# Kernel tuning notes

Hardware: AMD Instinct MI355X
Metric: run time of the kernel (lower is better)

Reference implementation:

```python
import jax, jax.numpy as jnp
import numpy as np

# Fixed architecture constants from AlgelogicNetwork.__init__
M, J, I, L, W = 4, 2, 3, 2, 9
B = 1048576  # batch size (only free dim)


def setup_inputs() -> dict:
    key = jax.random.key(0)
    ks = jax.random.split(key, 7)
    state = jax.random.normal(ks[0], (B, W * L), dtype=jnp.float32)
    # rule.constants ~ U(-1, 1), rule.gammas ~ U(0, 1), stacked over M rules
    constants = jax.random.uniform(ks[1], (M, J, L), minval=-1.0, maxval=1.0, dtype=jnp.float32)
    gammas = jax.random.uniform(ks[2], (M, J, L), dtype=jnp.float32)
    # body Linears (L -> I), one per (rule m, premise j); head Linear (I -> L) per rule
    W_body = jax.random.normal(ks[3], (M, J, I, L), dtype=jnp.float32) * 0.5
    b_body = jax.random.normal(ks[4], (M, J, I), dtype=jnp.float32) * 0.1
    W_head = jax.random.normal(ks[5], (M, L, I), dtype=jnp.float32) * 0.5
    b_head = jax.random.normal(ks[6], (M, L), dtype=jnp.float32) * 0.1
    return {
        "state": state,
        "constants": constants,
        "gammas": gammas,
        "W_body": W_body,
        "b_body": b_body,
        "W_head": W_head,
        "b_head": b_head,
    }


def reference(state, constants, gammas, W_body, b_body, W_head, b_head):
    s = state.reshape(-1, W, L)                       # [B, W, L]
    g = jnp.clip(gammas, 0.0, 1.0)                    # sigmoid() in source = clamp; [M, J, L]
    wgt = 1.0 - g                                     # [M, J, L]

    # match_scores[m,j,b,w] = sum_l (1-g[m,j,l]) * (const[m,j,l] - s[b,w,l])^2
    # L=2 fixed: unroll over l to avoid a [M,J,B,W,L] intermediate
    ms = sum(
        wgt[:, :, l, None, None]
        * (constants[:, :, l, None, None] - s[None, None, :, :, l]) ** 2
        for l in range(L)
    )                                                  # [M, J, B, W]

    attn = jax.nn.softmax(-ms, axis=-1)                # softmax over W positions (temperature=1)
    best = jnp.einsum('mjbw,bwl->mjbl', attn, s)       # soft-gathered propositions
    match_quality = jnp.sum(attn * ms, axis=-1).sum(axis=1)   # [M, B], summed over premises j

    captured = jnp.einsum('mjbl,mjil->mjbi', best, W_body) + b_body[:, :, None, :]  # body Linear
    g_avg = g.mean(axis=-1)                            # [M, J]
    captured_vars = jnp.einsum('mj,mjbi->mbi', g_avg, captured)                     # [M, B, I]

    rule_out = jnp.einsum('mbi,mli->mbl', captured_vars, W_head) + b_head[:, None, :]  # [M, B, L]

    # similarity[m,b,w] = -sum_l (rule_out[m,b,l] - s[b,w,l])^2
    sim = -jnp.sum((rule_out[:, :, None, :] - s[None]) ** 2, axis=-1)  # [M, B, W]
    confidence = jnp.exp(-match_quality)               # [M, B]
    return jnp.einsum('mb,mbw->bw', confidence, sim)   # [B, W]
```

## Files before the change

### kernel.cpp

```cpp
#include <hip/hip_runtime.h>

namespace {
constexpr int kM = 4, kJ = 2, kI = 3, kL = 2, kW = 9;
constexpr float kInvLn2 = 1.4426950408889634f;

__device__ __forceinline__ float fexp2(float x) { return __builtin_amdgcn_exp2f(x); }

__global__ __launch_bounds__(256) void algelogic_one(
    const float* __restrict__ state,
    const float* __restrict__ constants,
    const float* __restrict__ gammas,
    const float* __restrict__ W_body,
    const float* __restrict__ b_body,
    const float* __restrict__ W_head,
    const float* __restrict__ b_head,
    float* __restrict__ out) {
  __shared__ float sdp[80];
  const int t = threadIdx.x;
  const int b = blockIdx.x * 256 + t;

  const float2* sr = reinterpret_cast<const float2*>(state) + (size_t)b * kW;
  float s0[kW], s1[kW];
#pragma unroll
  for (int w = 0; w < kW; ++w) {
    const float2 v = sr[w];
    s0[w] = v.x; s1[w] = v.y;
  }

  if (t < 8) {
    const int mj = t, m = t >> 1, j = t & 1;
    const float g0 = fminf(fmaxf(gammas[mj * kL + 0], 0.f), 1.f);
    const float g1 = fminf(fmaxf(gammas[mj * kL + 1], 0.f), 1.f);
    const float w0 = 1.f - g0, w1 = 1.f - g1;
    const float c0 = constants[mj * kL + 0], c1 = constants[mj * kL + 1];
    const float gavg = 0.5f * (g0 + g1);
    float* base = sdp + m * 20;
    base[0 + j] = -(w0 * c0 * c0 + w1 * c1 * c1) * kInvLn2;
    base[2 + j] = 2.f * w0 * c0 * kInvLn2;
    base[4 + j] = 2.f * w1 * c1 * kInvLn2;
    base[6 + j] = -w0 * kInvLn2;
    base[8 + j] = -w1 * kInvLn2;
#pragma unroll
    for (int l = 0; l < kL; ++l)
#pragma unroll
      for (int lp = 0; lp < kL; ++lp) {
        float acc = 0.f;
#pragma unroll
        for (int i = 0; i < kI; ++i)
          acc += W_head[(m * kL + l) * kI + i] * W_body[(mj * kI + i) * kL + lp];
        base[10 + (l * 2 + lp) * 2 + j] = gavg * acc;
      }
  } else if (t >= 64 && t < 68) {
    const int m = t - 64;
#pragma unroll
    for (int l = 0; l < kL; ++l) {
      float d = b_head[m * kL + l];
#pragma unroll
      for (int j = 0; j < kJ; ++j) {
        const int mj = m * kJ + j;
        const float g0 = fminf(fmaxf(gammas[mj * kL + 0], 0.f), 1.f);
        const float g1 = fminf(fmaxf(gammas[mj * kL + 1], 0.f), 1.f);
        const float gavg = 0.5f * (g0 + g1);
        float acc = 0.f;
#pragma unroll
        for (int i = 0; i < kI; ++i)
          acc += W_head[(m * kL + l) * kI + i] * b_body[mj * kI + i];
        d += gavg * acc;
      }
      sdp[m * 20 + 18 + l] = d;
    }
  }
  __syncthreads();

  float Cs = 0.f, X0 = 0.f, X1 = 0.f, K = 0.f;

#pragma unroll 1
  for (int m = 0; m < kM; ++m) {
    const float4* P4 = reinterpret_cast<const float4*>(sdp + m * 20);
    const float4 f0 = P4[0], f1 = P4[1], f2 = P4[2], f3 = P4[3], f4 = P4[4];

    float p0 = 1e-35f, p1 = 1e-35f;
    float a0 = 0.f, a1 = 0.f;
    float b0 = 0.f, b1 = 0.f;
    float g0 = 0.f, g1 = 0.f;
#pragma unroll
    for (int w = 0; w < kW; ++w) {
      const float sx = s0[w], sy = s1[w];
      float u = fmaf(f1.z, sx, f0.z);
      float mN0 = fmaf(u, sx, f0.x);
      float v = fmaf(f2.x, sy, f1.x);
      mN0 = fmaf(v, sy, mN0);
      const float e0 = fexp2(mN0);
      p0 += e0;
      a0 = fmaf(e0, sx, a0);
      b0 = fmaf(e0, sy, b0);
      g0 = fmaf(e0, mN0, g0);
      float u1 = fmaf(f1.w, sx, f0.w);
      float mN1 = fmaf(u1, sx, f0.y);
      float v1 = fmaf(f2.y, sy, f1.y);
      mN1 = fmaf(v1, sy, mN1);
      const float e1 = fexp2(mN1);
      p1 += e1;
      a1 = fmaf(e1, sx, a1);
      b1 = fmaf(e1, sy, b1);
      g1 = fmaf(e1, mN1, g1);
    }

    const float i0 = __builtin_amdgcn_rcpf(p0);
    const float i1 = __builtin_amdgcn_rcpf(p1);
    const float bb00 = a0 * i0, bb10 = b0 * i0;
    const float bb01 = a1 * i1, bb11 = b1 * i1;
    const float mq2 = fmaf(g0, i0, g1 * i1);
    const float conf = fexp2(mq2);

    float r0 = fmaf(f2.z, bb00, f4.z);
    r0 = fmaf(f3.x, bb10, r0);
    r0 = fmaf(f2.w, bb01, r0);
    r0 = fmaf(f3.y, bb11, r0);
    float r1 = fmaf(f3.z, bb00, f4.w);
    r1 = fmaf(f4.x, bb10, r1);
    r1 = fmaf(f3.w, bb01, r1);
    r1 = fmaf(f4.y, bb11, r1);

    Cs += conf;
    X0 = fmaf(conf, r0, X0);
    X1 = fmaf(conf, r1, X1);
    K = fmaf(conf, fmaf(r0, r0, r1 * r1), K);
  }

  const float X02 = 2.f * X0, X12 = 2.f * X1;
  float* orow = out + (size_t)b * kW;
#pragma unroll
  for (int w = 0; w < kW; ++w) {
    const float sx = s0[w], sy = s1[w];
    const float qs = fmaf(sx, sx, sy * sy);
    orow[w] = fmaf(X02, sx, fmaf(X12, sy, fmaf(-Cs, qs, -K)));
  }
}
}

extern "C" void kernel_launch(void* const* d_in, const int* in_sizes, int n_in,
                              void* d_out, int out_size, void* d_ws, size_t ws_size,
                              hipStream_t stream) {
  const float* state     = (const float*)d_in[0];
  const float* constants = (const float*)d_in[1];
  const float* gammas    = (const float*)d_in[2];
  const float* W_body    = (const float*)d_in[3];
  const float* b_body    = (const float*)d_in[4];
  const float* W_head    = (const float*)d_in[5];
  const float* b_head    = (const float*)d_in[6];
  float* out = (float*)d_out;

  const int B = in_sizes[0] / (kW * kL);
  hipLaunchKernelGGL(algelogic_one, dim3(B / 256), dim3(256), 0, stream,
                     state, constants, gammas, W_body, b_body, W_head, b_head, out);
}
```

Baseline: 32.92 us.

## Process two batch rows per thread with float4 loads and float2 stores

Each thread now handles a pair of batch rows, reading their 36 floats as nine float4 loads and writing outputs as float2 stores instead of float2 loads and scalar stores. The intent is wider memory transactions and half as many threads, so the per-block parameter setup is amortised over more work. In exchange, each thread holds more registers and the grid shrinks to half the blocks, which may reduce occupancy and latency hiding.

Result: slower. 37.42 us (+13.6%).

```diff
diff --git a/kernel.cpp b/kernel.cpp
--- a/kernel.cpp
+++ b/kernel.cpp
@@ -6,7 +6,7 @@
 
 __device__ __forceinline__ float fexp2(float x) { return __builtin_amdgcn_exp2f(x); }
 
-__global__ __launch_bounds__(256) void algelogic_one(
+__global__ __launch_bounds__(256) void algelogic_pair(
     const float* __restrict__ state,
     const float* __restrict__ constants,
     const float* __restrict__ gammas,
@@ -17,15 +17,12 @@
     float* __restrict__ out) {
   __shared__ float sdp[80];
   const int t = threadIdx.x;
-  const int b = blockIdx.x * 256 + t;
+  const size_t pi = (size_t)blockIdx.x * 256 + t;
 
-  const float2* sr = reinterpret_cast<const float2*>(state) + (size_t)b * kW;
-  float s0[kW], s1[kW];
+  const float4* sq = reinterpret_cast<const float4*>(state) + pi * 9;
+  float4 sF[9];
 #pragma unroll
-  for (int w = 0; w < kW; ++w) {
-    const float2 v = sr[w];
-    s0[w] = v.x; s1[w] = v.y;
-  }
+  for (int k = 0; k < 9; ++k) sF[k] = sq[k];
 
   if (t < 8) {
     const int mj = t, m = t >> 1, j = t & 1;
@@ -72,69 +69,98 @@
   }
   __syncthreads();
 
-  float Cs = 0.f, X0 = 0.f, X1 = 0.f, K = 0.f;
+  float Cs[2] = {0.f, 0.f}, X0[2] = {0.f, 0.f}, X1[2] = {0.f, 0.f},
+        K[2] = {0.f, 0.f};
 
 #pragma unroll 1
   for (int m = 0; m < kM; ++m) {
     const float4* P4 = reinterpret_cast<const float4*>(sdp + m * 20);
     const float4 f0 = P4[0], f1 = P4[1], f2 = P4[2], f3 = P4[3], f4 = P4[4];
 
-    float p0 = 1e-35f, p1 = 1e-35f;
-    float a0 = 0.f, a1 = 0.f;
-    float b0 = 0.f, b1 = 0.f;
-    float g0 = 0.f, g1 = 0.f;
+#pragma unroll
+    for (int elem = 0; elem < 2; ++elem) {
+      float p0 = 1e-35f, p1 = 1e-35f;
+      float a0 = 0.f, a1 = 0.f;
+      float b0 = 0.f, b1 = 0.f;
+      float q0 = 0.f, q1 = 0.f;
+#pragma unroll
+      for (int w = 0; w < kW; ++w) {
+        const int g = elem * 9 + w;
+        const float4 f = sF[g >> 1];
+        const float sx = (g & 1) ? f.z : f.x;
+        const float sy = (g & 1) ? f.w : f.y;
+        float u = fmaf(f1.z, sx, f0.z);
+        float mN0 = fmaf(u, sx, f0.x);
+        float v = fmaf(f2.x, sy, f1.x);
+        mN0 = fmaf(v, sy, mN0);
+        const float e0 = fexp2(mN0);
+        p0 += e0;
+        a0 = fmaf(e0, sx, a0);
+        b0 = fmaf(e0, sy, b0);
+        q0 = fmaf(e0, mN0, q0);
+        float u1 = fmaf(f1.w, sx, f0.w);
+        float mN1 = fmaf(u1, sx, f0.y);
+        float v1 = fmaf(f2.y, sy, f1.y);
+        mN1 = fmaf(v1, sy, mN1);
+        const float e1 = fexp2(mN1);
+        p1 += e1;
+        a1 = fmaf(e1, sx, a1);
+        b1 = fmaf(e1, sy, b1);
+        q1 = fmaf(e1, mN1, q1);
+      }
+
+      const float i0 = __builtin_amdgcn_rcpf(p0);
+      const float i1 = __builtin_amdgcn_rcpf(p1);
+      const float bb00 = a0 * i0, bb10 = b0 * i0;
+      const float bb01 = a1 * i1, bb11 = b1 * i1;
+      const float mq2 = fmaf(q0, i0, q1 * i1);
+      const float conf = fexp2(mq2);
+
+      float r0 = fmaf(f2.z, bb00, f4.z);
+      r0 = fmaf(f3.x, bb10, r0);
+      r0 = fmaf(f2.w, bb01, r0);
+      r0 = fmaf(f3.y, bb11, r0);
+      float r1 = fmaf(f3.z, bb00, f4.w);
+      r1 = fmaf(f4.x, bb10, r1);
+      r1 = fmaf(f3.w, bb01, r1);
+      r1 = fmaf(f4.y, bb11, r1);
+
+      Cs[elem] += conf;
+      X0[elem] = fmaf(conf, r0, X0[elem]);
+      X1[elem] = fmaf(conf, r1, X1[elem]);
+      K[elem] = fmaf(conf, fmaf(r0, r0, r1 * r1), K[elem]);
+    }
+  }
+
+  float* orow = out + pi * (2 * kW);
+#pragma unroll
+  for (int elem = 0; elem < 2; ++elem) {
+    const float X02 = 2.f * X0[elem], X12 = 2.f * X1[elem];
+    const float Csl = Cs[elem], Kl = K[elem];
+    float o[kW];
 #pragma unroll
     for (int w = 0; w < kW; ++w) {
-      const float sx = s0[w], sy = s1[w];
-      float u = fmaf(f1.z, sx, f0.z);
-      float mN0 = fmaf(u, sx, f0.x);
-      float v = fmaf(f2.x, sy, f1.x);
-      mN0 = fmaf(v, sy, mN0);
-      const float e0 = fexp2(mN0);
-      p0 += e0;
-      a0 = fmaf(e0, sx, a0);
-      b0 = fmaf(e0, sy, b0);
-      g0 = fmaf(e0, mN0, g0);
-      float u1 = fmaf(f1.w, sx, f0.w);
-      float mN1 = fmaf(u1, sx, f0.y);
-      float v1 = fmaf(f2.y, sy, f1.y);
-      mN1 = fmaf(v1, sy, mN1);
-      const float e1 = fexp2(mN1);
-      p1 += e1;
-      a1 = fmaf(e1, sx, a1);
-      b1 = fmaf(e1, sy, b1);
-      g1 = fmaf(e1, mN1, g1);
+      const int g = elem * 9 + w;
+      const float4 f = sF[g >> 1];
+      const float sx = (g & 1) ? f.z : f.x;
+      const float sy = (g & 1) ? f.w : f.y;
+      const float qs = fmaf(sx, sx, sy * sy);
+      o[w] = fmaf(X02, sx, fmaf(X12, sy, fmaf(-Csl, qs, -Kl)));
     }
-
-    const float i0 = __builtin_amdgcn_rcpf(p0);
-    const float i1 = __builtin_amdgcn_rcpf(p1);
-    const float bb00 = a0 * i0, bb10 = b0 * i0;
-    const float bb01 = a1 * i1, bb11 = b1 * i1;
-    const float mq2 = fmaf(g0, i0, g1 * i1);
-    const float conf = fexp2(mq2);
-
-    float r0 = fmaf(f2.z, bb00, f4.z);
-    r0 = fmaf(f3.x, bb10, r0);
-    r0 = fmaf(f2.w, bb01, r0);
-    r0 = fmaf(f3.y, bb11, r0);
-    float r1 = fmaf(f3.z, bb00, f4.w);
-    r1 = fmaf(f4.x, bb10, r1);
-    r1 = fmaf(f3.w, bb01, r1);
-    r1 = fmaf(f4.y, bb11, r1);
-
-    Cs += conf;
-    X0 = fmaf(conf, r0, X0);
-    X1 = fmaf(conf, r1, X1);
-    K = fmaf(conf, fmaf(r0, r0, r1 * r1), K);
-  }
-
-  const float X02 = 2.f * X0, X12 = 2.f * X1;
-  float* orow = out + (size_t)b * kW;
-#pragma unroll
-  for (int w = 0; w < kW; ++w) {
-    const float sx = s0[w], sy = s1[w];
-    const float qs = fmaf(sx, sx, sy * sy);
-    orow[w] = fmaf(X02, sx, fmaf(X12, sy, fmaf(-Cs, qs, -K)));
+    float* base = orow + elem * kW;
+    if (elem == 0) {
+      *reinterpret_cast<float2*>(base + 0) = make_float2(o[0], o[1]);
+      *reinterpret_cast<float2*>(base + 2) = make_float2(o[2], o[3]);
+      *reinterpret_cast<float2*>(base + 4) = make_float2(o[4], o[5]);
+      *reinterpret_cast<float2*>(base + 6) = make_float2(o[6], o[7]);
+      base[8] = o[8];
+    } else {
+      base[0] = o[0];
+      *reinterpret_cast<float2*>(base + 1) = make_float2(o[1], o[2]);
+      *reinterpret_cast<float2*>(base + 3) = make_float2(o[3], o[4]);
+      *reinterpret_cast<float2*>(base + 5) = make_float2(o[5], o[6]);
+      *reinterpret_cast<float2*>(base + 7) = make_float2(o[7], o[8]);
+    }
   }
 }
 }
@@ -152,6 +178,7 @@
   float* out = (float*)d_out;
 
   const int B = in_sizes[0] / (kW * kL);
-  hipLaunchKernelGGL(algelogic_one, dim3(B / 256), dim3(256), 0, stream,
+  const int pairs = B / 2;
+  hipLaunchKernelGGL(algelogic_pair, dim3(pairs / 256), dim3(256), 0, stream,
                      state, constants, gammas, W_body, b_body, W_head, b_head, out);
 }
```
